# Performance work log

Hardware: AMD Instinct MI355X
Metric: run time of the kernel (lower is better)

## Reference

```python
import jax, jax.numpy as jnp
import numpy as np

K = 3  # kernel size (hardcoded in module defaults; padding=1, stride=1, dilation=1)


def conv2d(x, w, b, pad=1):
    # x: [B,C,H,W], w: [O,C,kh,kw]
    out = jax.lax.conv_general_dilated(
        x, w, window_strides=(1, 1), padding=[(pad, pad), (pad, pad)],
        dimension_numbers=("NCHW", "OIHW", "NCHW"))
    return out + b[None, :, None, None]


def _bilinear_sample(img, py, px):
    # img: [C,H,W]; py, px: [K*K,Ho,Wo] float sample coords.
    # Zero-padded bilinear sampling (matches torchvision deform_conv2d):
    # each of the 4 corner taps contributes 0 if it lies outside the image.
    H, W = img.shape[1], img.shape[2]
    y0 = jnp.floor(py)
    x0 = jnp.floor(px)
    y1, x1 = y0 + 1.0, x0 + 1.0
    wy1 = py - y0
    wy0 = 1.0 - wy1
    wx1 = px - x0
    wx0 = 1.0 - wx1

    def corner(y, x):
        yi = jnp.clip(y.astype(jnp.int32), 0, H - 1)
        xi = jnp.clip(x.astype(jnp.int32), 0, W - 1)
        valid = ((y >= 0) & (y <= H - 1) & (x >= 0) & (x <= W - 1))
        return img[:, yi, xi] * valid.astype(img.dtype)[None]  # [C,K*K,Ho,Wo]

    return (corner(y0, x0) * (wy0 * wx0)[None]
            + corner(y0, x1) * (wy0 * wx1)[None]
            + corner(y1, x0) * (wy1 * wx0)[None]
            + corner(y1, x1) * (wy1 * wx1)[None])


def setup_inputs() -> dict:
    key = jax.random.key(0)
    ks = jax.random.split(key, 4)
    B, C, O, H, W = 8, 128, 256, 96, 96
    x = jax.random.normal(ks[0], (B, C, H, W), dtype=jnp.float32)
    # scale offset/mask conv weights so learned offsets stay a few pixels
    offset_w = jax.random.normal(ks[1], (2 * K * K, C, K, K), dtype=jnp.float32) * 0.01
    offset_b = jnp.zeros((2 * K * K,), dtype=jnp.float32)
    mask_w = jax.random.normal(ks[2], (K * K, C, K, K), dtype=jnp.float32) * 0.05
    mask_b = jnp.zeros((K * K,), dtype=jnp.float32)
    weight = jax.random.normal(ks[3], (O, C, K, K), dtype=jnp.float32) * 0.05
    bias = jnp.zeros((O,), dtype=jnp.float32)
    return {"x": x, "offset_w": offset_w, "offset_b": offset_b,
            "mask_w": mask_w, "mask_b": mask_b, "weight": weight, "bias": bias}


def reference(x, offset_w, offset_b, mask_w, mask_b, weight, bias):
    B, C, H, W = x.shape
    O = weight.shape[0]
    pad = 1
    offset = conv2d(x, offset_w, offset_b, pad)              # [B,2*K*K,H,W]
    mask = jax.nn.sigmoid(conv2d(x, mask_w, mask_b, pad))    # [B,K*K,H,W]
    Ho, Wo = offset.shape[2], offset.shape[3]

    # base sampling grid: output pixel - pad + kernel tap position
    kh, kw = jnp.meshgrid(jnp.arange(K), jnp.arange(K), indexing="ij")
    kh = kh.reshape(-1).astype(x.dtype)  # [K*K]
    kw = kw.reshape(-1).astype(x.dtype)
    base_y = (jnp.arange(Ho, dtype=x.dtype)[None, :, None] - pad
              + kh[:, None, None])                           # [K*K,Ho,1]
    base_x = (jnp.arange(Wo, dtype=x.dtype)[None, None, :] - pad
              + kw[:, None, None])                           # [K*K,1,Wo]

    # torchvision layout: channel 2k = y-offset, 2k+1 = x-offset for tap k
    off = offset.reshape(B, K * K, 2, Ho, Wo)
    py = base_y[None] + off[:, :, 0]                         # [B,K*K,Ho,Wo]
    px = base_x[None] + off[:, :, 1]

    samples = jax.vmap(_bilinear_sample)(x, py, px)          # [B,C,K*K,Ho,Wo]
    w_flat = weight.reshape(O, C, K * K)
    out = jnp.einsum("bckhw,bkhw,ock->bohw", samples, mask, w_flat)
    return out + bias[None, :, None, None]
```

## Files before the change

### kernel.cpp

```cpp
#include <hip/hip_runtime.h>

#define CIN 128
#define COUT 256
#define IH 96
#define IW 96
#define NB 8
#define HW (IH*IW)
#define NPIX (NB*HW)
#define AST 136
#define BLK_PER_IMG (HW/64)

typedef __attribute__((ext_vector_type(8))) short short8;
typedef __attribute__((ext_vector_type(4))) float floatx4;

static __device__ __forceinline__ short f2bf(float f) {
  unsigned int u = __builtin_bit_cast(unsigned int, f);
  u = u + 0x7fffu + ((u >> 16) & 1u);
  return (short)(u >> 16);
}
static __device__ __forceinline__ float bf2f(short s) {
  unsigned int u = ((unsigned int)(unsigned short)s) << 16;
  return __builtin_bit_cast(float, u);
}

struct Corner {
  float w00, w01, w10, w11;
  const short *r00, *r01, *r10, *r11;
};

static __device__ __forceinline__ Corner corner_setup(float py, float px, float mk,
                                                      const short* xtb, int choff) {
  Corner c;
  float y0f = floorf(py), x0f = floorf(px);
  float wy1 = py - y0f, wx1 = px - x0f;
  float wy0 = 1.f - wy1, wx0 = 1.f - wx1;
  bool vy0 = (y0f >= 0.f) && (y0f <= (float)(IH - 1));
  bool vy1 = (y0f + 1.f >= 0.f) && (y0f + 1.f <= (float)(IH - 1));
  bool vx0 = (x0f >= 0.f) && (x0f <= (float)(IW - 1));
  bool vx1 = (x0f + 1.f >= 0.f) && (x0f + 1.f <= (float)(IW - 1));
  int iy0 = min(max((int)y0f, 0), IH - 1);
  int iy1 = min(max((int)y0f + 1, 0), IH - 1);
  int ix0 = min(max((int)x0f, 0), IW - 1);
  int ix1 = min(max((int)x0f + 1, 0), IW - 1);
  c.w00 = wy0 * wx0 * mk * ((vy0 && vx0) ? 1.f : 0.f);
  c.w01 = wy0 * wx1 * mk * ((vy0 && vx1) ? 1.f : 0.f);
  c.w10 = wy1 * wx0 * mk * ((vy1 && vx0) ? 1.f : 0.f);
  c.w11 = wy1 * wx1 * mk * ((vy1 && vx1) ? 1.f : 0.f);
  c.r00 = xtb + (size_t)(iy0 * IW + ix0) * 128 + choff;
  c.r01 = xtb + (size_t)(iy0 * IW + ix1) * 128 + choff;
  c.r10 = xtb + (size_t)(iy1 * IW + ix0) * 128 + choff;
  c.r11 = xtb + (size_t)(iy1 * IW + ix1) * 128 + choff;
  return c;
}

static __device__ __forceinline__ short8 interp8(short8 s00, short8 s01,
                                                 short8 s10, short8 s11,
                                                 const Corner& c) {
  short8 o;
  #pragma unroll
  for (int j = 0; j < 8; ++j) {
    float v = c.w00 * bf2f(s00[j]) + c.w01 * bf2f(s01[j])
            + c.w10 * bf2f(s10[j]) + c.w11 * bf2f(s11[j]);
    o[j] = f2bf(v);
  }
  return o;
}

__global__ void prep_weights(const float* __restrict__ weight,
                             const float* __restrict__ offset_w,
                             const float* __restrict__ mask_w,
                             short* __restrict__ Bt2f,
                             short* __restrict__ Bt1f) {
  int idx = blockIdx.x * 256 + threadIdx.x;
  const int n2 = 9 * 4 * 16 * 512;
  if (idx < n2) {
    int e = idx & 7, lane = (idx >> 3) & 63;
    int g = idx >> 9;
    int nl = g & 15, kq = (g >> 4) & 3, tap = g >> 6;
    int o = nl * 16 + (lane & 15);
    int c = kq * 32 + (lane >> 4) * 8 + e;
    Bt2f[idx] = f2bf(weight[(o * CIN + c) * 9 + tap]);
  } else {
    int j = idx - n2;
    if (j < 9 * 4 * 2 * 512) {
      int e = j & 7, lane = (j >> 3) & 63;
      int g = j >> 9;
      int nl = g & 1, kq = (g >> 1) & 3, tap = g >> 3;
      int n = nl * 16 + (lane & 15);
      int c = kq * 32 + (lane >> 4) * 8 + e;
      float v = 0.f;
      if (n < 27)
        v = (n < 18) ? offset_w[(n * CIN + c) * 9 + tap]
                     : mask_w[((n - 18) * CIN + c) * 9 + tap];
      Bt1f[j] = f2bf(v);
    }
  }
}

__global__ __launch_bounds__(256, 8)
void transpose_x(const float* __restrict__ x, short* __restrict__ xt) {
  __shared__ short tile[64 * 130];
  const int tid = threadIdx.x;
  const int lane = tid & 63;
  const int wv = tid >> 6;
  const int p0 = blockIdx.x * 64;
  const int b = p0 / HW;
  const int hw0 = p0 % HW;
  const float* xb = x + (size_t)b * CIN * HW + hw0;

  #pragma unroll
  for (int i = 0; i < 32; ++i) {
    int c = wv + i * 4;
    tile[lane * 130 + c] = f2bf(xb[(size_t)c * HW + lane]);
  }
  __syncthreads();

  unsigned int* dst = (unsigned int*)(xt + ((size_t)b * HW + hw0) * 128);
  #pragma unroll
  for (int i = 0; i < 16; ++i) {
    int idx = i * 256 + tid;
    int px = idx >> 6, cw = idx & 63;
    unsigned int lo = (unsigned short)tile[px * 130 + 2 * cw];
    unsigned int hi = (unsigned short)tile[px * 130 + 2 * cw + 1];
    dst[idx] = lo | (hi << 16);
  }
}

__global__ __launch_bounds__(256, 4)
void offmask_kernel(const short* __restrict__ xt,
                    const short* __restrict__ Bt1f,
                    const float* __restrict__ offset_b,
                    const float* __restrict__ mask_b,
                    float* __restrict__ pmt) {
  const int tid  = threadIdx.x;
  const int lane = tid & 63;
  const int wv   = tid >> 6;
  const int q    = lane >> 4;
  const int m    = lane & 15;
  const int blk  = blockIdx.x;
  const int l    = (blk & 7) * BLK_PER_IMG + (blk >> 3);
  const int p0   = l * 64;
  const int b    = p0 / HW;
  const int p    = p0 + wv * 16 + m;
  const int hw   = p % HW;
  const int h    = hw / IW, w_ = hw % IW;
  const short* xtb = xt + (size_t)b * HW * 128;

  floatx4 acc0 = (floatx4){0.f, 0.f, 0.f, 0.f};
  floatx4 acc1 = (floatx4){0.f, 0.f, 0.f, 0.f};

  for (int tap = 0; tap < 9; ++tap) {
    const int kh = tap / 3, kw = tap % 3;
    const int iy = h + kh - 1, ix = w_ + kw - 1;
    const bool vald = (iy >= 0 && iy < IH && ix >= 0 && ix < IW);
    const size_t pbase = vald ? (size_t)(iy * IW + ix) * 128 : 0;

    short8 a[4], bb0[4], bb1[4];
    #pragma unroll
    for (int kq = 0; kq < 4; ++kq)
      a[kq] = *(const short8*)(xtb + pbase + kq * 32 + q * 8);
    #pragma unroll
    for (int kq = 0; kq < 4; ++kq) {
      bb0[kq] = *(const short8*)(Bt1f + (size_t)((tap * 4 + kq) * 2 + 0) * 512 + lane * 8);
      bb1[kq] = *(const short8*)(Bt1f + (size_t)((tap * 4 + kq) * 2 + 1) * 512 + lane * 8);
    }
    #pragma unroll
    for (int kq = 0; kq < 4; ++kq) {
      short8 av = a[kq];
      if (!vald) av = (short8){0, 0, 0, 0, 0, 0, 0, 0};
      acc0 = __builtin_amdgcn_mfma_f32_16x16x32_bf16(av, bb0[kq], acc0, 0, 0, 0);
      acc1 = __builtin_amdgcn_mfma_f32_16x16x32_bf16(av, bb1[kq], acc1, 0, 0, 0);
    }
  }

  #pragma unroll
  for (int nl = 0; nl < 2; ++nl) {
    floatx4 ac = nl ? acc1 : acc0;
    int ch = nl * 16 + m;
    if (ch < 18) {
      int tap = ch >> 1, plane = ch & 1;
      float cb = offset_b[ch];
      #pragma unroll
      for (int r = 0; r < 4; ++r) {
        int pp = p0 + wv * 16 + q * 4 + r;
        int hwp = pp % HW;
        float base = plane ? (float)(hwp % IW + tap % 3 - 1)
                           : (float)(hwp / IW + tap / 3 - 1);
        pmt[(size_t)(plane * 9 + tap) * NPIX + pp] = ac[r] + cb + base;
      }
    } else if (ch < 27) {
      int tap = ch - 18;
      float cb = mask_b[tap];
      #pragma unroll
      for (int r = 0; r < 4; ++r) {
        int pp = p0 + wv * 16 + q * 4 + r;
        float v = ac[r] + cb;
        pmt[(size_t)(18 + tap) * NPIX + pp] = 1.f / (1.f + expf(-v));
      }
    }
  }
}

__global__ __launch_bounds__(256, 3)
void deform_main(const short* __restrict__ xt,
                 const short* __restrict__ Bt2f,
                 const float* __restrict__ pmt,
                 const float* __restrict__ bias,
                 float* __restrict__ out) {
  __shared__ short Ald[2][64 * AST];

  const int tid  = threadIdx.x;
  const int lane = tid & 63;
  const int wv   = tid >> 6;
  const int q    = lane >> 4;
  const int m    = lane & 15;
  const int blk  = blockIdx.x;
  const int l    = (blk & 7) * BLK_PER_IMG + (blk >> 3);
  const int p0   = l * 64;
  const int b    = p0 / HW;
  const short* xtb = xt + (size_t)b * HW * 128;

  const int spx   = lane;
  const int p_s   = p0 + spx;
  const int choff = wv * 32;
  const int wsw   = spx & 3;
  const int rsw   = m & 3;
  short* const myrow0 = &Ald[0][spx * AST];
  short* const myrow1 = &Ald[1][spx * AST];

  floatx4 acc[4][4];
  #pragma unroll
  for (int i = 0; i < 4; ++i)
    #pragma unroll
    for (int j = 0; j < 4; ++j) acc[i][j] = (floatx4){0.f, 0.f, 0.f, 0.f};

  {
    float py = pmt[p_s];
    float px = pmt[(size_t)9 * NPIX + p_s];
    float mk = pmt[(size_t)18 * NPIX + p_s];
    Corner c = corner_setup(py, px, mk, xtb, choff);
    #pragma unroll
    for (int i = 0; i < 4; ++i) {
      short8 s00 = *(const short8*)(c.r00 + i * 8);
      short8 s01 = *(const short8*)(c.r01 + i * 8);
      short8 s10 = *(const short8*)(c.r10 + i * 8);
      short8 s11 = *(const short8*)(c.r11 + i * 8);
      *(short8*)(myrow0 + ((wv * 4 + i) ^ wsw) * 8) = interp8(s00, s01, s10, s11, c);
    }
  }
  float pyN = pmt[(size_t)1 * NPIX + p_s];
  float pxN = pmt[(size_t)10 * NPIX + p_s];
  float mkN = pmt[(size_t)19 * NPIX + p_s];
  __syncthreads();

  for (int tap = 0; tap < 9; ++tap) {
    const short* bufr = Ald[tap & 1];
    short* const roww = (tap & 1) ? myrow0 : myrow1;
    const bool nxt = (tap < 8);

    Corner c;
    if (nxt) c = corner_setup(pyN, pxN, mkN, xtb, choff);
    if (tap < 7) {
      pyN = pmt[(size_t)(tap + 2) * NPIX + p_s];
      pxN = pmt[(size_t)(tap + 11) * NPIX + p_s];
      mkN = pmt[(size_t)(tap + 20) * NPIX + p_s];
    }

    short8 gp00, gp01, gp10, gp11;
    #pragma unroll
    for (int kq = 0; kq < 4; ++kq) {
      short8 bf[4];
      #pragma unroll
      for (int nl = 0; nl < 4; ++nl)
        bf[nl] = *(const short8*)(Bt2f + (size_t)((tap * 4 + kq) * 16 + wv * 4 + nl) * 512 + lane * 8);
      short8 g00, g01, g10, g11;
      if (nxt) {
        g00 = *(const short8*)(c.r00 + kq * 8);
        g01 = *(const short8*)(c.r01 + kq * 8);
        g10 = *(const short8*)(c.r10 + kq * 8);
        g11 = *(const short8*)(c.r11 + kq * 8);
      }
      short8 af[4];
      #pragma unroll
      for (int mt = 0; mt < 4; ++mt)
        af[mt] = *(const short8*)(bufr + (mt * 16 + m) * AST + ((kq * 4 + q) ^ rsw) * 8);
      #pragma unroll
      for (int mt = 0; mt < 4; ++mt)
        #pragma unroll
        for (int nl = 0; nl < 4; ++nl)
          acc[mt][nl] = __builtin_amdgcn_mfma_f32_16x16x32_bf16(af[mt], bf[nl], acc[mt][nl], 0, 0, 0);
      if (nxt && kq > 0)
        *(short8*)(roww + ((wv * 4 + kq - 1) ^ wsw) * 8) = interp8(gp00, gp01, gp10, gp11, c);
      gp00 = g00; gp01 = g01; gp10 = g10; gp11 = g11;
    }
    if (nxt) {
      *(short8*)(roww + ((wv * 4 + 3) ^ wsw) * 8) = interp8(gp00, gp01, gp10, gp11, c);
      __syncthreads();
    }
  }

  const int hw0 = p0 % HW;
  #pragma unroll
  for (int nl = 0; nl < 4; ++nl) {
    const int o = wv * 64 + nl * 16 + m;
    const float bs = bias[o];
    float* op = out + (size_t)(b * COUT + o) * HW + hw0;
    #pragma unroll
    for (int mt = 0; mt < 4; ++mt) {
      floatx4 v = acc[mt][nl];
      v[0] += bs; v[1] += bs; v[2] += bs; v[3] += bs;
      *(floatx4*)(op + mt * 16 + q * 4) = v;
    }
  }
}

extern "C" void kernel_launch(void* const* d_in, const int* in_sizes, int n_in,
                              void* d_out, int out_size, void* d_ws, size_t ws_size,
                              hipStream_t stream) {
  const float* x        = (const float*)d_in[0];
  const float* offset_w = (const float*)d_in[1];
  const float* offset_b = (const float*)d_in[2];
  const float* mask_w   = (const float*)d_in[3];
  const float* mask_b   = (const float*)d_in[4];
  const float* weight   = (const float*)d_in[5];
  const float* bias     = (const float*)d_in[6];
  float* out = (float*)d_out;

  char* ws = (char*)d_ws;
  const size_t XT_BYTES  = (size_t)NPIX * 128 * 2;
  const size_t PMT_BYTES = (size_t)27 * NPIX * 4;
  const size_t BT2_BYTES = (size_t)9 * 4 * 16 * 512 * 2;
  short* xtp  = (short*)ws;
  float* pmt  = (float*)(ws + XT_BYTES);
  short* Bt2f = (short*)(ws + XT_BYTES + PMT_BYTES);
  short* Bt1f = (short*)(ws + XT_BYTES + PMT_BYTES + BT2_BYTES);

  prep_weights<<<dim3(1296), dim3(256), 0, stream>>>(weight, offset_w, mask_w, Bt2f, Bt1f);
  transpose_x<<<dim3(NPIX / 64), dim3(256), 0, stream>>>(x, xtp);
  offmask_kernel<<<dim3(NPIX / 64), dim3(256), 0, stream>>>(xtp, Bt1f, offset_b, mask_b, pmt);
  deform_main<<<dim3(NPIX / 64), dim3(256), 0, stream>>>(xtp, Bt2f, pmt, bias, out);
}
```

Before: 258.4 us.

## Restructure deform tap loop into two-stage gather batches with wider LDS swizzle

The per-tap inner loop is manually restructured so B-fragment loads and corner gathers are issued two k-chunks at a time, giving memory loads more MFMA work to hide behind before the interpolated rows are written to LDS. The LDS XOR swizzle widens from 2 bits to 3 bits of (row>>1) to cut bank conflicts on the A-fragment reads and row writes. Launch bounds drop from 3 to 2 blocks per CU so the kernel can hold more live registers for the larger prefetch set. This trades occupancy for more in-flight loads per wave.

```diff
diff --git a/kernel.cpp b/kernel.cpp
--- a/kernel.cpp
+++ b/kernel.cpp
@@ -201,7 +201,7 @@
   }
 }
 
-__global__ __launch_bounds__(256, 3)
+__global__ __launch_bounds__(256, 2)
 void deform_main(const short* __restrict__ xt,
                  const short* __restrict__ Bt2f,
                  const float* __restrict__ pmt,
@@ -223,8 +223,8 @@
   const int spx   = lane;
   const int p_s   = p0 + spx;
   const int choff = wv * 32;
-  const int wsw   = spx & 3;
-  const int rsw   = m & 3;
+  const int wsw   = (spx >> 1) & 7;
+  const int rsw   = (m >> 1) & 7;
   short* const myrow0 = &Ald[0][spx * AST];
   short* const myrow1 = &Ald[1][spx * AST];
 
@@ -266,35 +266,80 @@
       mkN = pmt[(size_t)(tap + 20) * NPIX + p_s];
     }
 
-    short8 gp00, gp01, gp10, gp11;
-    #pragma unroll
-    for (int kq = 0; kq < 4; ++kq) {
-      short8 bf[4];
-      #pragma unroll
-      for (int nl = 0; nl < 4; ++nl)
-        bf[nl] = *(const short8*)(Bt2f + (size_t)((tap * 4 + kq) * 16 + wv * 4 + nl) * 512 + lane * 8);
-      short8 g00, g01, g10, g11;
-      if (nxt) {
-        g00 = *(const short8*)(c.r00 + kq * 8);
-        g01 = *(const short8*)(c.r01 + kq * 8);
-        g10 = *(const short8*)(c.r10 + kq * 8);
-        g11 = *(const short8*)(c.r11 + kq * 8);
-      }
+    short8 bfA[4], bfB[4];
+    #pragma unroll
+    for (int nl = 0; nl < 4; ++nl) {
+      bfA[nl] = *(const short8*)(Bt2f + (size_t)((tap * 4 + 0) * 16 + wv * 4 + nl) * 512 + lane * 8);
+      bfB[nl] = *(const short8*)(Bt2f + (size_t)((tap * 4 + 1) * 16 + wv * 4 + nl) * 512 + lane * 8);
+    }
+    short8 gA0, gA1, gA2, gA3, gB0, gB1, gB2, gB3;
+    if (nxt) {
+      gA0 = *(const short8*)(c.r00 + 0);  gA1 = *(const short8*)(c.r01 + 0);
+      gA2 = *(const short8*)(c.r10 + 0);  gA3 = *(const short8*)(c.r11 + 0);
+      gB0 = *(const short8*)(c.r00 + 8);  gB1 = *(const short8*)(c.r01 + 8);
+      gB2 = *(const short8*)(c.r10 + 8);  gB3 = *(const short8*)(c.r11 + 8);
+    }
+    {
       short8 af[4];
       #pragma unroll
       for (int mt = 0; mt < 4; ++mt)
-        af[mt] = *(const short8*)(bufr + (mt * 16 + m) * AST + ((kq * 4 + q) ^ rsw) * 8);
+        af[mt] = *(const short8*)(bufr + (mt * 16 + m) * AST + ((0 * 4 + q) ^ rsw) * 8);
       #pragma unroll
       for (int mt = 0; mt < 4; ++mt)
         #pragma unroll
         for (int nl = 0; nl < 4; ++nl)
-          acc[mt][nl] = __builtin_amdgcn_mfma_f32_16x16x32_bf16(af[mt], bf[nl], acc[mt][nl], 0, 0, 0);
-      if (nxt && kq > 0)
-        *(short8*)(roww + ((wv * 4 + kq - 1) ^ wsw) * 8) = interp8(gp00, gp01, gp10, gp11, c);
-      gp00 = g00; gp01 = g01; gp10 = g10; gp11 = g11;
+          acc[mt][nl] = __builtin_amdgcn_mfma_f32_16x16x32_bf16(af[mt], bfA[nl], acc[mt][nl], 0, 0, 0);
+    }
+    {
+      short8 af[4];
+      #pragma unroll
+      for (int mt = 0; mt < 4; ++mt)
+        af[mt] = *(const short8*)(bufr + (mt * 16 + m) * AST + ((1 * 4 + q) ^ rsw) * 8);
+      #pragma unroll
+      for (int mt = 0; mt < 4; ++mt)
+        #pragma unroll
+        for (int nl = 0; nl < 4; ++nl)
+          acc[mt][nl] = __builtin_amdgcn_mfma_f32_16x16x32_bf16(af[mt], bfB[nl], acc[mt][nl], 0, 0, 0);
+    }
+    short8 bfC[4], bfD[4];
+    #pragma unroll
+    for (int nl = 0; nl < 4; ++nl) {
+      bfC[nl] = *(const short8*)(Bt2f + (size_t)((tap * 4 + 2) * 16 + wv * 4 + nl) * 512 + lane * 8);
+      bfD[nl] = *(const short8*)(Bt2f + (size_t)((tap * 4 + 3) * 16 + wv * 4 + nl) * 512 + lane * 8);
     }
     if (nxt) {
-      *(short8*)(roww + ((wv * 4 + 3) ^ wsw) * 8) = interp8(gp00, gp01, gp10, gp11, c);
+      *(short8*)(roww + ((wv * 4 + 0) ^ wsw) * 8) = interp8(gA0, gA1, gA2, gA3, c);
+      *(short8*)(roww + ((wv * 4 + 1) ^ wsw) * 8) = interp8(gB0, gB1, gB2, gB3, c);
+      gA0 = *(const short8*)(c.r00 + 16);  gA1 = *(const short8*)(c.r01 + 16);
+      gA2 = *(const short8*)(c.r10 + 16);  gA3 = *(const short8*)(c.r11 + 16);
+      gB0 = *(const short8*)(c.r00 + 24);  gB1 = *(const short8*)(c.r01 + 24);
+      gB2 = *(const short8*)(c.r10 + 24);  gB3 = *(const short8*)(c.r11 + 24);
+    }
+    {
+      short8 af[4];
+      #pragma unroll
+      for (int mt = 0; mt < 4; ++mt)
+        af[mt] = *(const short8*)(bufr + (mt * 16 + m) * AST + ((2 * 4 + q) ^ rsw) * 8);
+      #pragma unroll
+      for (int mt = 0; mt < 4; ++mt)
+        #pragma unroll
+        for (int nl = 0; nl < 4; ++nl)
+          acc[mt][nl] = __builtin_amdgcn_mfma_f32_16x16x32_bf16(af[mt], bfC[nl], acc[mt][nl], 0, 0, 0);
+    }
+    {
+      short8 af[4];
+      #pragma unroll
+      for (int mt = 0; mt < 4; ++mt)
+        af[mt] = *(const short8*)(bufr + (mt * 16 + m) * AST + ((3 * 4 + q) ^ rsw) * 8);
+      #pragma unroll
+      for (int mt = 0; mt < 4; ++mt)
+        #pragma unroll
+        for (int nl = 0; nl < 4; ++nl)
+          acc[mt][nl] = __builtin_amdgcn_mfma_f32_16x16x32_bf16(af[mt], bfD[nl], acc[mt][nl], 0, 0, 0);
+    }
+    if (nxt) {
+      *(short8*)(roww + ((wv * 4 + 2) ^ wsw) * 8) = interp8(gA0, gA1, gA2, gA3, c);
+      *(short8*)(roww + ((wv * 4 + 3) ^ wsw) * 8) = interp8(gB0, gB1, gB2, gB3, c);
       __syncthreads();
     }
   }
```

New measurement: 257.3 us. About the same (-0.4%).
